# Optimization experiments

Hardware: AMD Instinct MI355X
Metric: run time of the kernel (lower is better)

Reference implementation:

```python
import jax, jax.numpy as jnp
import numpy as np

B, H, S, D = 2, 8, 2048, 64

def setup_inputs() -> dict:
    key = jax.random.key(0)
    ks = jax.random.split(key, 6)
    names = ["Qx", "Kx", "Vx", "Qy", "Ky", "Vy"]
    return {n: jax.random.normal(k, (B, H, S, D), dtype=jnp.float32)
            for n, k in zip(names, ks)}

def reference(Qx, Kx, Vx, Qy, Ky, Vy):
    scale = float(np.sqrt(Qx.shape[-1]))
    # Two score matmuls: [B,H,S,S] each
    ax = jnp.einsum('bhqd,bhkd->bhqk', Qx, Kx)
    ay = jnp.einsum('bhqd,bhkd->bhqk', Qy, Ky)
    # cat(dim=1) -> reshape(B,2,H,S,S) -> mean(dim=1) == elementwise average
    attn = (ax + ay) * 0.5
    # numerically stable softmax over keys; dropout is identity in eval mode
    w = jax.nn.softmax(attn / scale, axis=-1)
    # Shared attention weights into two value matmuls
    out1 = jnp.einsum('bhqk,bhkd->bhqd', w, Vx)
    out2 = jnp.einsum('bhqk,bhkd->bhqd', w, Vy)
    return (out1, out2)
```

## Files before the change

### kernel.cpp

```cpp
#include <hip/hip_runtime.h>
#include <hip/hip_bf16.h>

typedef __attribute__((ext_vector_type(4)))  float f32x4;
typedef __attribute__((ext_vector_type(16))) float f32x16;
typedef __attribute__((ext_vector_type(8)))  short s16x8;
typedef __attribute__((ext_vector_type(4)))  short s16x4;
typedef __attribute__((ext_vector_type(4)))  int   i32x4;

#define BB 2
#define HH 8
#define SS 2048
#define DD 64
#define QBLK 128
#define KBLK 64
#define NT   (SS / KBLK)
#define NBH  (BB * HH)

#define WS_KX 0
#define WS_KY ((size_t)NBH * NT * 8192)
#define WS_VX ((size_t)2 * NBH * NT * 8192)
#define WS_VY ((size_t)3 * NBH * NT * 8192)
#define WS_NEED ((size_t)4 * NBH * NT * 8192)

__device__ __forceinline__ short f2bf(float x) {
    unsigned u = __builtin_bit_cast(unsigned, x);
    u = (u + 0x7FFFu + ((u >> 16) & 1u)) >> 16;
    return (short)u;
}

__device__ __forceinline__ unsigned cvtpk(float lo, float hi) {
    unsigned d;
    asm("v_cvt_pk_bf16_f32 %0, %1, %2" : "=v"(d) : "v"(lo), "v"(hi));
    return d;
}

__device__ __forceinline__ int swz(int row, int byteInRow) {
    return row * 128 + (byteInRow ^ ((row & 7) << 4));
}

__device__ __forceinline__ void glds16(const void* g, void* l) {
    __builtin_amdgcn_global_load_lds(
        (const __attribute__((address_space(1))) unsigned*)g,
        (__attribute__((address_space(3))) unsigned*)l, 16, 0, 0);
}

__global__ __launch_bounds__(256)
void prep_k(const float* __restrict__ Kx, const float* __restrict__ Ky,
            char* __restrict__ ws)
{
    const int tid  = blockIdx.x * 256 + threadIdx.x;
    const int dblk = tid & 7;
    const int s    = (tid >> 3) & 2047;
    const int bh   = tid >> 14;
    const size_t gi = ((size_t)bh * SS + s) * DD + dblk * 8;
    const int kt = s >> 6, row = s & 63;
    const size_t dst = (size_t)(bh * NT + kt) * 8192 + swz(row, dblk * 16);

    const float* px = Kx + gi;
    const float* py = Ky + gi;
    s16x8 a, b;
#pragma unroll
    for (int i = 0; i < 8; ++i) { a[i] = f2bf(px[i]); b[i] = f2bf(py[i]); }
    *(s16x8*)(ws + WS_KX + dst) = a;
    *(s16x8*)(ws + WS_KY + dst) = b;
}

__global__ __launch_bounds__(256)
void prep_v(const float* __restrict__ Vx, const float* __restrict__ Vy,
            char* __restrict__ ws)
{
    const int tid  = blockIdx.x * 256 + threadIdx.x;
    const int d    = tid & 63;
    const int sblk = (tid >> 6) & 7;
    const int kt   = (tid >> 9) & 31;
    const int bh   = tid >> 14;
    const size_t gbase = ((size_t)bh * SS + kt * 64 + sblk * 8) * DD + d;
    s16x8 a, b;
#pragma unroll
    for (int i = 0; i < 8; ++i) {
        a[i] = f2bf(Vx[gbase + (size_t)i * DD]);
        b[i] = f2bf(Vy[gbase + (size_t)i * DD]);
    }
    const size_t dst = (size_t)(bh * NT + kt) * 8192 + swz(d, sblk * 16);
    *(s16x8*)(ws + WS_VX + dst) = a;
    *(s16x8*)(ws + WS_VY + dst) = b;
}

__global__ __launch_bounds__(512, 2)
void attn_main(const float* __restrict__ Qx, const float* __restrict__ Qy,
               const char* __restrict__ ws, float* __restrict__ Out)
{
    extern __shared__ char lds[];

    const int t    = threadIdx.x;
    const int lane = t & 63;
    const int w    = t >> 6;
    const int qsub = w & 3;
    const int ks   = w >> 2;
    const int l31  = lane & 31;
    const int hi   = lane >> 5;

    int bid = blockIdx.x;
    bid = (bid & 7) * 32 + (bid >> 3);
    const int bh = bid >> 4;
    const int q0 = (bid & 15) * QBLK;
    const size_t base = (size_t)bh * SS * DD;

    const int qrow = q0 + qsub * 32 + l31;
    s16x8 qbx[4], qby[4];
#pragma unroll
    for (int dc = 0; dc < 4; ++dc) {
        const int d0 = dc * 16 + hi * 8;
        const float* qp = Qx + base + (size_t)qrow * DD + d0;
        const float* qq = Qy + base + (size_t)qrow * DD + d0;
        const float4 f0 = *(const float4*)qp;
        const float4 f1 = *(const float4*)(qp + 4);
        const float4 h0 = *(const float4*)qq;
        const float4 h1 = *(const float4*)(qq + 4);
        qbx[dc][0]=f2bf(f0.x); qbx[dc][1]=f2bf(f0.y); qbx[dc][2]=f2bf(f0.z); qbx[dc][3]=f2bf(f0.w);
        qbx[dc][4]=f2bf(f1.x); qbx[dc][5]=f2bf(f1.y); qbx[dc][6]=f2bf(f1.z); qbx[dc][7]=f2bf(f1.w);
        qby[dc][0]=f2bf(h0.x); qby[dc][1]=f2bf(h0.y); qby[dc][2]=f2bf(h0.z); qby[dc][3]=f2bf(h0.w);
        qby[dc][4]=f2bf(h1.x); qby[dc][5]=f2bf(h1.y); qby[dc][6]=f2bf(h1.z); qby[dc][7]=f2bf(h1.w);
    }

    f32x16 o1[2], o2[2];
#pragma unroll
    for (int dt = 0; dt < 2; ++dt)
#pragma unroll
        for (int j = 0; j < 16; ++j) { o1[dt][j] = 0.f; o2[dt][j] = 0.f; }
    float lsum = 0.f;

    const float SCL = 0.09016844005556021f;

#define STAGE(kt_, b_)                                                             \
    do {                                                                           \
        const size_t img_ = (size_t)(bh * NT + (kt_)) * 8192 + (size_t)t * 16;     \
        char* dst_ = lds + (b_) * 32768 + t * 16;                                  \
        glds16(ws + WS_KX + img_, dst_);                                           \
        glds16(ws + WS_KY + img_, dst_ + 8192);                                    \
        glds16(ws + WS_VX + img_, dst_ + 16384);                                   \
        glds16(ws + WS_VY + img_, dst_ + 24576);                                   \
    } while (0)

    STAGE(0, 0);
    __syncthreads();
    int cur = 0;

    for (int kt = 0; kt < NT; ++kt) {
        if (kt + 1 < NT) STAGE(kt + 1, cur ^ 1);

        const char* KxL = lds + cur * 32768;
        const char* KyL = KxL + 8192;
        const char* VxL = KxL + 16384;
        const char* VyL = KxL + 24576;

        f32x16 sc;
#pragma unroll
        for (int j = 0; j < 16; ++j) sc[j] = 0.f;
#pragma unroll
        for (int dc = 0; dc < 4; ++dc) {
            const int off = swz(ks * 32 + l31, dc * 32 + hi * 16);
            const s16x8 ka = *(const s16x8*)(KxL + off);
            const s16x8 kb = *(const s16x8*)(KyL + off);
            sc = __builtin_amdgcn_mfma_f32_32x32x16_bf16(ka, qbx[dc], sc, 0, 0, 0);
            sc = __builtin_amdgcn_mfma_f32_32x32x16_bf16(kb, qby[dc], sc, 0, 0, 0);
        }

        float p[16];
        float s = 0.f;
#pragma unroll
        for (int j = 0; j < 16; ++j) {
            p[j] = exp2f(sc[j] * SCL);
            s += p[j];
        }
        lsum += s;

        s16x8 pa[2];
#pragma unroll
        for (int ch = 0; ch < 2; ++ch) {
            const int b = ch * 8;
            const unsigned x0 = cvtpk(p[b + 0], p[b + 1]);
            const unsigned x1 = cvtpk(p[b + 2], p[b + 3]);
            const unsigned y0 = cvtpk(p[b + 4], p[b + 5]);
            const unsigned y1 = cvtpk(p[b + 6], p[b + 7]);
            const unsigned xs0 = (unsigned)__shfl_xor((int)x0, 32);
            const unsigned xs1 = (unsigned)__shfl_xor((int)x1, 32);
            const unsigned ys0 = (unsigned)__shfl_xor((int)y0, 32);
            const unsigned ys1 = (unsigned)__shfl_xor((int)y1, 32);
            i32x4 pw;
            pw[0] = (int)(hi ? ys0 : x0);
            pw[1] = (int)(hi ? ys1 : x1);
            pw[2] = (int)(hi ? y0 : xs0);
            pw[3] = (int)(hi ? y1 : xs1);
            pa[ch] = __builtin_bit_cast(s16x8, pw);
        }

#pragma unroll
        for (int dt = 0; dt < 2; ++dt) {
#pragma unroll
            for (int ch = 0; ch < 2; ++ch) {
                const int off = swz(dt * 32 + l31, ks * 64 + ch * 32 + hi * 16);
                const s16x8 vxf = *(const s16x8*)(VxL + off);
                const s16x8 vyf = *(const s16x8*)(VyL + off);
                o1[dt] = __builtin_amdgcn_mfma_f32_32x32x16_bf16(pa[ch], vxf, o1[dt], 0, 0, 0);
                o2[dt] = __builtin_amdgcn_mfma_f32_32x32x16_bf16(pa[ch], vyf, o2[dt], 0, 0, 0);
            }
        }

        __syncthreads();
        cur ^= 1;
    }
#undef STAGE

    float lh = lsum + __shfl_xor(lsum, 32);

    __syncthreads();
    float* ex   = (float*)lds;
    float* invA = (float*)(lds + 40960);
    const int exo = (qsub * 64 + lane) * 33;

    if (ks == 1) {
#pragma unroll
        for (int dt = 0; dt < 2; ++dt)
#pragma unroll
            for (int j = 0; j < 16; ++j) ex[exo + dt * 16 + j] = o1[dt][j];
        ex[exo + 32] = lh;
    }
    __syncthreads();

    float* O1 = Out;
    float* O2 = Out + (size_t)BB * HH * SS * DD;

    if (ks == 0) {
        const float ltot = lh + ex[exo + 32];
        if (lane < 32) invA[qsub * 32 + l31] = 1.0f / ltot;
    }
    __syncthreads();

    if (ks == 0) {
#pragma unroll
        for (int j = 0; j < 16; ++j) {
            const int qr = (j & 3) + 8 * (j >> 2) + 4 * hi;
            const float invj = invA[qsub * 32 + qr];
            const size_t ob = base + (size_t)(q0 + qsub * 32 + qr) * DD + l31;
            O1[ob]      = (o1[0][j] + ex[exo + j])      * invj;
            O1[ob + 32] = (o1[1][j] + ex[exo + 16 + j]) * invj;
        }
    }
    __syncthreads();

    if (ks == 1) {
#pragma unroll
        for (int dt = 0; dt < 2; ++dt)
#pragma unroll
            for (int j = 0; j < 16; ++j) ex[exo + dt * 16 + j] = o2[dt][j];
    }
    __syncthreads();

    if (ks == 0) {
#pragma unroll
        for (int j = 0; j < 16; ++j) {
            const int qr = (j & 3) + 8 * (j >> 2) + 4 * hi;
            const float invj = invA[qsub * 32 + qr];
            const size_t ob = base + (size_t)(q0 + qsub * 32 + qr) * DD + l31;
            O2[ob]      = (o2[0][j] + ex[exo + j])      * invj;
            O2[ob + 32] = (o2[1][j] + ex[exo + 16 + j]) * invj;
        }
    }
}

__global__ __launch_bounds__(256, 2)
void attn_dual_fallback(const float* __restrict__ Qx, const float* __restrict__ Kx,
                        const float* __restrict__ Vx, const float* __restrict__ Qy,
                        const float* __restrict__ Ky, const float* __restrict__ Vy,
                        float* __restrict__ Out)
{
    __shared__ __attribute__((aligned(16))) char lds[40960];
    char* KxL  = lds;
    char* KyL  = lds + 8192;
    char* VtxL = lds + 16384;
    char* VtyL = lds + 24576;

    const int t    = threadIdx.x;
    const int lane = t & 63;
    const int w    = t >> 6;
    const int g    = lane >> 4;
    const int c    = lane & 15;
    char* PL = lds + 32768 + w * 2048;

    const int bid = blockIdx.x;
    const int bh  = bid >> 5;
    const int q0  = (bid & 31) * 64;
    const size_t base = (size_t)bh * SS * DD;

    const int qrowA = q0 + w * 16 + c;
    s16x8 qxf[2], qyf[2];
#pragma unroll
    for (int kk = 0; kk < 2; ++kk) {
        const int d0 = kk * 32 + g * 8;
        const float* qp = Qx + base + (size_t)qrowA * DD + d0;
        const float* qq = Qy + base + (size_t)qrowA * DD + d0;
#pragma unroll
        for (int i = 0; i < 8; ++i) { qxf[kk][i] = f2bf(qp[i]); qyf[kk][i] = f2bf(qq[i]); }
    }

    f32x4 o1[4], o2[4];
#pragma unroll
    for (int n = 0; n < 4; ++n) {
        o1[n] = (f32x4){0.f, 0.f, 0.f, 0.f};
        o2[n] = (f32x4){0.f, 0.f, 0.f, 0.f};
    }
    float m[4]    = {-1e30f, -1e30f, -1e30f, -1e30f};
    float lsum[4] = {0.f, 0.f, 0.f, 0.f};
    const float SCL = 0.09016844005556021f;

    for (int kt = 0; kt < SS / 64; ++kt) {
        __syncthreads();
#pragma unroll
        for (int j = 0; j < 4; ++j) {
            const int f   = t + 256 * j;
            const int row = f >> 4;
            const int c4  = f & 15;
            const size_t gi = base + (size_t)(kt * 64 + row) * DD + c4 * 4;
            const float4 kx = *(const float4*)(Kx + gi);
            const float4 ky = *(const float4*)(Ky + gi);
            const float4 vx = *(const float4*)(Vx + gi);
            const float4 vy = *(const float4*)(Vy + gi);
            s16x4 a; a[0]=f2bf(kx.x); a[1]=f2bf(kx.y); a[2]=f2bf(kx.z); a[3]=f2bf(kx.w);
            *(s16x4*)(KxL + swz(row, c4 * 8)) = a;
            s16x4 b; b[0]=f2bf(ky.x); b[1]=f2bf(ky.y); b[2]=f2bf(ky.z); b[3]=f2bf(ky.w);
            *(s16x4*)(KyL + swz(row, c4 * 8)) = b;
            const int d0 = c4 * 4;
            *(short*)(VtxL + swz(d0 + 0, row * 2)) = f2bf(vx.x);
            *(short*)(VtxL + swz(d0 + 1, row * 2)) = f2bf(vx.y);
            *(short*)(VtxL + swz(d0 + 2, row * 2)) = f2bf(vx.z);
            *(short*)(VtxL + swz(d0 + 3, row * 2)) = f2bf(vx.w);
            *(short*)(VtyL + swz(d0 + 0, row * 2)) = f2bf(vy.x);
            *(short*)(VtyL + swz(d0 + 1, row * 2)) = f2bf(vy.y);
            *(short*)(VtyL + swz(d0 + 2, row * 2)) = f2bf(vy.z);
            *(short*)(VtyL + swz(d0 + 3, row * 2)) = f2bf(vy.w);
        }
        __syncthreads();

        f32x4 sc[4];
#pragma unroll
        for (int n = 0; n < 4; ++n) {
            f32x4 acc = (f32x4){0.f, 0.f, 0.f, 0.f};
            const int keyrow = n * 16 + c;
#pragma unroll
            for (int kk = 0; kk < 2; ++kk) {
                const int off = swz(keyrow, (kk * 32 + g * 8) * 2);
                const s16x8 kxf = *(const s16x8*)(KxL + off);
                const s16x8 kyf = *(const s16x8*)(KyL + off);
                acc = __builtin_amdgcn_mfma_f32_16x16x32_bf16(qxf[kk], kxf, acc, 0, 0, 0);
                acc = __builtin_amdgcn_mfma_f32_16x16x32_bf16(qyf[kk], kyf, acc, 0, 0, 0);
            }
            sc[n] = acc;
        }

#pragma unroll
        for (int r = 0; r < 4; ++r) {
            float v0 = fmaxf(fmaxf(sc[0][r], sc[1][r]), fmaxf(sc[2][r], sc[3][r])) * SCL;
#pragma unroll
            for (int off = 1; off < 16; off <<= 1) v0 = fmaxf(v0, __shfl_xor(v0, off));
            const float mnew = fmaxf(m[r], v0);
            const float cr = exp2f(m[r] - mnew);
            m[r] = mnew;
            float srow = 0.f;
#pragma unroll
            for (int n = 0; n < 4; ++n) {
                const float pp = exp2f(sc[n][r] * SCL - mnew);
                srow += pp;
                *(short*)(PL + swz(g * 4 + r, (n * 16 + c) * 2)) = f2bf(pp);
            }
#pragma unroll
            for (int off = 1; off < 16; off <<= 1) srow += __shfl_xor(srow, off);
            lsum[r] = lsum[r] * cr + srow;
#pragma unroll
            for (int n = 0; n < 4; ++n) { o1[n][r] *= cr; o2[n][r] *= cr; }
        }

        s16x8 pf[2];
#pragma unroll
        for (int kk = 0; kk < 2; ++kk)
            pf[kk] = *(const s16x8*)(PL + swz(c, (kk * 32 + g * 8) * 2));
#pragma unroll
        for (int nd = 0; nd < 4; ++nd) {
            const int drow = nd * 16 + c;
#pragma unroll
            for (int kk = 0; kk < 2; ++kk) {
                const int off = swz(drow, (kk * 32 + g * 8) * 2);
                const s16x8 vxf = *(const s16x8*)(VtxL + off);
                const s16x8 vyf = *(const s16x8*)(VtyL + off);
                o1[nd] = __builtin_amdgcn_mfma_f32_16x16x32_bf16(pf[kk], vxf, o1[nd], 0, 0, 0);
                o2[nd] = __builtin_amdgcn_mfma_f32_16x16x32_bf16(pf[kk], vyf, o2[nd], 0, 0, 0);
            }
        }
    }

    float* O1 = Out;
    float* O2 = Out + (size_t)BB * HH * SS * DD;
#pragma unroll
    for (int r = 0; r < 4; ++r) {
        const float inv = 1.0f / lsum[r];
        const int qrow = q0 + w * 16 + g * 4 + r;
        const size_t ob = base + (size_t)qrow * DD + c;
#pragma unroll
        for (int nd = 0; nd < 4; ++nd) {
            O1[ob + nd * 16] = o1[nd][r] * inv;
            O2[ob + nd * 16] = o2[nd][r] * inv;
        }
    }
}

extern "C" void kernel_launch(void* const* d_in, const int* in_sizes, int n_in,
                              void* d_out, int out_size, void* d_ws, size_t ws_size,
                              hipStream_t stream) {
    const float* Qx = (const float*)d_in[0];
    const float* Kx = (const float*)d_in[1];
    const float* Vx = (const float*)d_in[2];
    const float* Qy = (const float*)d_in[3];
    const float* Ky = (const float*)d_in[4];
    const float* Vy = (const float*)d_in[5];
    float* Out = (float*)d_out;

    if (ws_size >= WS_NEED) {
        char* ws = (char*)d_ws;
        hipLaunchKernelGGL(prep_k, dim3(1024), dim3(256), 0, stream, Kx, Ky, ws);
        hipLaunchKernelGGL(prep_v, dim3(1024), dim3(256), 0, stream, Vx, Vy, ws);
        hipFuncSetAttribute((const void*)attn_main,
                            hipFuncAttributeMaxDynamicSharedMemorySize, 65536);
        hipLaunchKernelGGL(attn_main, dim3(NBH * (SS / QBLK)), dim3(512), 65536,
                           stream, Qx, Qy, (const char*)ws, Out);
    } else {
        hipLaunchKernelGGL(attn_dual_fallback, dim3(NBH * 32), dim3(256),
                           0, stream, Qx, Kx, Vx, Qy, Ky, Vy, Out);
    }
}
```

Measured before the change: 68.96 us.

## Halve query tile, split output D across warps, merge prep kernels

Query block size drops from 128 to 64, which doubles the grid to 512 blocks. Each warp now owns one 32-wide half of the output D dimension, so it keeps two accumulators instead of four and the key-split reduction epilogue runs in a single pass. The K and V bf16 prep kernels are fused into one launch, and s_setprio hints are placed around the MFMA sections. The smaller tiles spread work over more CUs and cut register pressure, at the cost of recomputing the QK scores twice per query tile (once for each D-half warp) and loading K/V tiles more often. Launch bounds now ask for 4 blocks per CU, but the 64 KB of dynamic LDS per block may not allow that.

New measurement: 92.41 us. +34.0%, slower.

```diff
diff --git a/kernel.cpp b/kernel.cpp
--- a/kernel.cpp
+++ b/kernel.cpp
@@ -11,7 +11,7 @@
 #define HH 8
 #define SS 2048
 #define DD 64
-#define QBLK 128
+#define QBLK 64
 #define KBLK 64
 #define NT   (SS / KBLK)
 #define NBH  (BB * HH)
@@ -45,48 +45,46 @@
 }
 
 __global__ __launch_bounds__(256)
-void prep_k(const float* __restrict__ Kx, const float* __restrict__ Ky,
-            char* __restrict__ ws)
+void prep_kv(const float* __restrict__ Kx, const float* __restrict__ Ky,
+             const float* __restrict__ Vx, const float* __restrict__ Vy,
+             char* __restrict__ ws)
 {
-    const int tid  = blockIdx.x * 256 + threadIdx.x;
-    const int dblk = tid & 7;
-    const int s    = (tid >> 3) & 2047;
-    const int bh   = tid >> 14;
-    const size_t gi = ((size_t)bh * SS + s) * DD + dblk * 8;
-    const int kt = s >> 6, row = s & 63;
-    const size_t dst = (size_t)(bh * NT + kt) * 8192 + swz(row, dblk * 16);
-
-    const float* px = Kx + gi;
-    const float* py = Ky + gi;
-    s16x8 a, b;
-#pragma unroll
-    for (int i = 0; i < 8; ++i) { a[i] = f2bf(px[i]); b[i] = f2bf(py[i]); }
-    *(s16x8*)(ws + WS_KX + dst) = a;
-    *(s16x8*)(ws + WS_KY + dst) = b;
-}
-
-__global__ __launch_bounds__(256)
-void prep_v(const float* __restrict__ Vx, const float* __restrict__ Vy,
-            char* __restrict__ ws)
-{
-    const int tid  = blockIdx.x * 256 + threadIdx.x;
-    const int d    = tid & 63;
-    const int sblk = (tid >> 6) & 7;
-    const int kt   = (tid >> 9) & 31;
-    const int bh   = tid >> 14;
-    const size_t gbase = ((size_t)bh * SS + kt * 64 + sblk * 8) * DD + d;
-    s16x8 a, b;
-#pragma unroll
-    for (int i = 0; i < 8; ++i) {
-        a[i] = f2bf(Vx[gbase + (size_t)i * DD]);
-        b[i] = f2bf(Vy[gbase + (size_t)i * DD]);
-    }
-    const size_t dst = (size_t)(bh * NT + kt) * 8192 + swz(d, sblk * 16);
-    *(s16x8*)(ws + WS_VX + dst) = a;
-    *(s16x8*)(ws + WS_VY + dst) = b;
-}
-
-__global__ __launch_bounds__(512, 2)
+    const int b = blockIdx.x;
+    if (b < 1024) {
+        const int tid  = b * 256 + threadIdx.x;
+        const int dblk = tid & 7;
+        const int s    = (tid >> 3) & 2047;
+        const int bh   = tid >> 14;
+        const size_t gi = ((size_t)bh * SS + s) * DD + dblk * 8;
+        const int kt = s >> 6, row = s & 63;
+        const size_t dst = (size_t)(bh * NT + kt) * 8192 + swz(row, dblk * 16);
+        const float* px = Kx + gi;
+        const float* py = Ky + gi;
+        s16x8 a, bb;
+#pragma unroll
+        for (int i = 0; i < 8; ++i) { a[i] = f2bf(px[i]); bb[i] = f2bf(py[i]); }
+        *(s16x8*)(ws + WS_KX + dst) = a;
+        *(s16x8*)(ws + WS_KY + dst) = bb;
+    } else {
+        const int tid  = (b - 1024) * 256 + threadIdx.x;
+        const int d    = tid & 63;
+        const int sblk = (tid >> 6) & 7;
+        const int kt   = (tid >> 9) & 31;
+        const int bh   = tid >> 14;
+        const size_t gbase = ((size_t)bh * SS + kt * 64 + sblk * 8) * DD + d;
+        s16x8 a, bb;
+#pragma unroll
+        for (int i = 0; i < 8; ++i) {
+            a[i]  = f2bf(Vx[gbase + (size_t)i * DD]);
+            bb[i] = f2bf(Vy[gbase + (size_t)i * DD]);
+        }
+        const size_t dst = (size_t)(bh * NT + kt) * 8192 + swz(d, sblk * 16);
+        *(s16x8*)(ws + WS_VX + dst) = a;
+        *(s16x8*)(ws + WS_VY + dst) = bb;
+    }
+}
+
+__global__ __launch_bounds__(512, 4)
 void attn_main(const float* __restrict__ Qx, const float* __restrict__ Qy,
                const char* __restrict__ ws, float* __restrict__ Out)
 {
@@ -95,15 +93,16 @@
     const int t    = threadIdx.x;
     const int lane = t & 63;
     const int w    = t >> 6;
-    const int qsub = w & 3;
-    const int ks   = w >> 2;
+    const int qsub = w & 1;
+    const int ks   = (w >> 1) & 1;
+    const int ds   = w >> 2;
     const int l31  = lane & 31;
     const int hi   = lane >> 5;
 
     int bid = blockIdx.x;
-    bid = (bid & 7) * 32 + (bid >> 3);
-    const int bh = bid >> 4;
-    const int q0 = (bid & 15) * QBLK;
+    bid = (bid & 7) * 64 + (bid >> 3);
+    const int bh = bid >> 5;
+    const int q0 = (bid & 31) * QBLK;
     const size_t base = (size_t)bh * SS * DD;
 
     const int qrow = q0 + qsub * 32 + l31;
@@ -123,11 +122,9 @@
         qby[dc][4]=f2bf(h1.x); qby[dc][5]=f2bf(h1.y); qby[dc][6]=f2bf(h1.z); qby[dc][7]=f2bf(h1.w);
     }
 
-    f32x16 o1[2], o2[2];
-#pragma unroll
-    for (int dt = 0; dt < 2; ++dt)
-#pragma unroll
-        for (int j = 0; j < 16; ++j) { o1[dt][j] = 0.f; o2[dt][j] = 0.f; }
+    f32x16 o1h, o2h;
+#pragma unroll
+    for (int j = 0; j < 16; ++j) { o1h[j] = 0.f; o2h[j] = 0.f; }
     float lsum = 0.f;
 
     const float SCL = 0.09016844005556021f;
@@ -157,6 +154,7 @@
         f32x16 sc;
 #pragma unroll
         for (int j = 0; j < 16; ++j) sc[j] = 0.f;
+        __builtin_amdgcn_s_setprio(1);
 #pragma unroll
         for (int dc = 0; dc < 4; ++dc) {
             const int off = swz(ks * 32 + l31, dc * 32 + hi * 16);
@@ -165,24 +163,24 @@
             sc = __builtin_amdgcn_mfma_f32_32x32x16_bf16(ka, qbx[dc], sc, 0, 0, 0);
             sc = __builtin_amdgcn_mfma_f32_32x32x16_bf16(kb, qby[dc], sc, 0, 0, 0);
         }
-
-        float p[16];
+        __builtin_amdgcn_s_setprio(0);
+
         float s = 0.f;
 #pragma unroll
         for (int j = 0; j < 16; ++j) {
-            p[j] = exp2f(sc[j] * SCL);
-            s += p[j];
+            sc[j] = exp2f(sc[j] * SCL);
+            s += sc[j];
         }
         lsum += s;
 
         s16x8 pa[2];
 #pragma unroll
         for (int ch = 0; ch < 2; ++ch) {
-            const int b = ch * 8;
-            const unsigned x0 = cvtpk(p[b + 0], p[b + 1]);
-            const unsigned x1 = cvtpk(p[b + 2], p[b + 3]);
-            const unsigned y0 = cvtpk(p[b + 4], p[b + 5]);
-            const unsigned y1 = cvtpk(p[b + 6], p[b + 7]);
+            const int b8 = ch * 8;
+            const unsigned x0 = cvtpk(sc[b8 + 0], sc[b8 + 1]);
+            const unsigned x1 = cvtpk(sc[b8 + 2], sc[b8 + 3]);
+            const unsigned y0 = cvtpk(sc[b8 + 4], sc[b8 + 5]);
+            const unsigned y1 = cvtpk(sc[b8 + 6], sc[b8 + 7]);
             const unsigned xs0 = (unsigned)__shfl_xor((int)x0, 32);
             const unsigned xs1 = (unsigned)__shfl_xor((int)x1, 32);
             const unsigned ys0 = (unsigned)__shfl_xor((int)y0, 32);
@@ -195,76 +193,52 @@
             pa[ch] = __builtin_bit_cast(s16x8, pw);
         }
 
-#pragma unroll
-        for (int dt = 0; dt < 2; ++dt) {
-#pragma unroll
-            for (int ch = 0; ch < 2; ++ch) {
-                const int off = swz(dt * 32 + l31, ks * 64 + ch * 32 + hi * 16);
-                const s16x8 vxf = *(const s16x8*)(VxL + off);
-                const s16x8 vyf = *(const s16x8*)(VyL + off);
-                o1[dt] = __builtin_amdgcn_mfma_f32_32x32x16_bf16(pa[ch], vxf, o1[dt], 0, 0, 0);
-                o2[dt] = __builtin_amdgcn_mfma_f32_32x32x16_bf16(pa[ch], vyf, o2[dt], 0, 0, 0);
-            }
-        }
+        __builtin_amdgcn_s_setprio(1);
+#pragma unroll
+        for (int ch = 0; ch < 2; ++ch) {
+            const int off = swz(ds * 32 + l31, ks * 64 + ch * 32 + hi * 16);
+            const s16x8 vxf = *(const s16x8*)(VxL + off);
+            const s16x8 vyf = *(const s16x8*)(VyL + off);
+            o1h = __builtin_amdgcn_mfma_f32_32x32x16_bf16(pa[ch], vxf, o1h, 0, 0, 0);
+            o2h = __builtin_amdgcn_mfma_f32_32x32x16_bf16(pa[ch], vyf, o2h, 0, 0, 0);
+        }
+        __builtin_amdgcn_s_setprio(0);
 
         __syncthreads();
         cur ^= 1;
     }
 #undef STAGE
 
-    float lh = lsum + __shfl_xor(lsum, 32);
-
+    const float lh = lsum + __shfl_xor(lsum, 32);
+
+    float* ex   = (float*)lds;
+    float* linv = (float*)(lds + 36864);
+    const int pid = qsub | (ds << 1);
+    const int exo = (pid * 64 + lane) * 35;
+
+    if (ks == 1) {
+#pragma unroll
+        for (int j = 0; j < 16; ++j) { ex[exo + j] = o1h[j]; ex[exo + 16 + j] = o2h[j]; }
+        ex[exo + 32] = lh;
+    }
     __syncthreads();
-    float* ex   = (float*)lds;
-    float* invA = (float*)(lds + 40960);
-    const int exo = (qsub * 64 + lane) * 33;
-
-    if (ks == 1) {
-#pragma unroll
-        for (int dt = 0; dt < 2; ++dt)
-#pragma unroll
-            for (int j = 0; j < 16; ++j) ex[exo + dt * 16 + j] = o1[dt][j];
-        ex[exo + 32] = lh;
+
+    if (ks == 0 && hi == 0) {
+        const float ltot = lh + ex[exo + 32];
+        linv[qsub * 32 + l31] = 1.0f / ltot;
     }
     __syncthreads();
 
-    float* O1 = Out;
-    float* O2 = Out + (size_t)BB * HH * SS * DD;
-
     if (ks == 0) {
-        const float ltot = lh + ex[exo + 32];
-        if (lane < 32) invA[qsub * 32 + l31] = 1.0f / ltot;
-    }
-    __syncthreads();
-
-    if (ks == 0) {
+        float* O1 = Out;
+        float* O2 = Out + (size_t)BB * HH * SS * DD;
 #pragma unroll
         for (int j = 0; j < 16; ++j) {
             const int qr = (j & 3) + 8 * (j >> 2) + 4 * hi;
-            const float invj = invA[qsub * 32 + qr];
-            const size_t ob = base + (size_t)(q0 + qsub * 32 + qr) * DD + l31;
-            O1[ob]      = (o1[0][j] + ex[exo + j])      * invj;
-            O1[ob + 32] = (o1[1][j] + ex[exo + 16 + j]) * invj;
-        }
-    }
-    __syncthreads();
-
-    if (ks == 1) {
-#pragma unroll
-        for (int dt = 0; dt < 2; ++dt)
-#pragma unroll
-            for (int j = 0; j < 16; ++j) ex[exo + dt * 16 + j] = o2[dt][j];
-    }
-    __syncthreads();
-
-    if (ks == 0) {
-#pragma unroll
-        for (int j = 0; j < 16; ++j) {
-            const int qr = (j & 3) + 8 * (j >> 2) + 4 * hi;
-            const float invj = invA[qsub * 32 + qr];
-            const size_t ob = base + (size_t)(q0 + qsub * 32 + qr) * DD + l31;
-            O2[ob]      = (o2[0][j] + ex[exo + j])      * invj;
-            O2[ob + 32] = (o2[1][j] + ex[exo + 16 + j]) * invj;
+            const float invj = linv[qsub * 32 + qr];
+            const size_t ob = base + (size_t)(q0 + qsub * 32 + qr) * DD + ds * 32 + l31;
+            O1[ob] = (o1h[j] + ex[exo + j])      * invj;
+            O2[ob] = (o2h[j] + ex[exo + 16 + j]) * invj;
         }
     }
 }
@@ -426,8 +400,8 @@
 
     if (ws_size >= WS_NEED) {
         char* ws = (char*)d_ws;
-        hipLaunchKernelGGL(prep_k, dim3(1024), dim3(256), 0, stream, Kx, Ky, ws);
-        hipLaunchKernelGGL(prep_v, dim3(1024), dim3(256), 0, stream, Vx, Vy, ws);
+        hipLaunchKernelGGL(prep_kv, dim3(2048), dim3(256), 0, stream,
+                           Kx, Ky, Vx, Vy, ws);
         hipFuncSetAttribute((const void*)attn_main,
                             hipFuncAttributeMaxDynamicSharedMemorySize, 65536);
         hipLaunchKernelGGL(attn_main, dim3(NBH * (SS / QBLK)), dim3(512), 65536,
```
